# Kernel tuning notes

Hardware: AMD Instinct MI355X
Metric: run time of the kernel (lower is better)

The kernel has to match this reference:

```python
import jax, jax.numpy as jnp
import numpy as np

N_NODES = 100000
N_EDGES = 6_400_000
IN_DIM = 128


def gcn_conv(x, W, b, row, col, ew):
    """PyG GCNConv(normalize=True, add_self_loops=True) forward."""
    n = x.shape[0]
    loop = jnp.arange(n)
    row_sl = jnp.concatenate([row, loop])
    col_sl = jnp.concatenate([col, loop])
    ew_sl = jnp.concatenate([ew, jnp.ones((n,), ew.dtype)])
    # symmetric normalization: deg^{-1/2}[src] * w * deg^{-1/2}[dst]
    deg = jax.ops.segment_sum(ew_sl, col_sl, num_segments=n)
    safe_deg = jnp.where(deg > 0, deg, 1.0)
    dis = jnp.where(deg > 0, jax.lax.rsqrt(safe_deg), 0.0)
    norm = dis[row_sl] * ew_sl * dis[col_sl]
    h = x @ W  # [n, out_dim] linear transform first (small out_dim)
    # gather source features, scale, scatter-add into targets
    out = jax.ops.segment_sum(norm[:, None] * h[row_sl], col_sl, num_segments=n)
    return out + b


def setup_inputs() -> dict:
    key = jax.random.key(0)
    ks = jax.random.split(key, 12)
    X = jax.random.normal(ks[0], (N_NODES, IN_DIM), dtype=jnp.float32)
    edge_index = jax.random.randint(ks[1], (2, N_EDGES), 0, N_NODES, dtype=jnp.int64)
    edge_weight = jax.random.uniform(ks[2], (N_EDGES,), dtype=jnp.float32)

    def glorot(k, fan_in, fan_out):
        lim = np.sqrt(6.0 / (fan_in + fan_out)).astype(np.float32)
        return jax.random.uniform(k, (fan_in, fan_out), minval=-lim, maxval=lim, dtype=jnp.float32)

    return {
        "X": X,
        "edge_index": edge_index,
        "edge_weight": edge_weight,
        "W1": glorot(ks[3], IN_DIM, 12), "b1": jnp.zeros((12,), jnp.float32),
        "W2": glorot(ks[4], 12, 6), "b2": jnp.zeros((6,), jnp.float32),
        "W3": glorot(ks[5], 6, 3), "b3": jnp.zeros((3,), jnp.float32),
        "Wl": glorot(ks[6], 3, 1), "bl": jnp.zeros((1,), jnp.float32),
    }


def reference(X, edge_index, edge_weight, W1, b1, W2, b2, W3, b3, Wl, bl):
    row, col = edge_index[0], edge_index[1]
    h = jax.nn.relu(gcn_conv(X, W1, b1, row, col, edge_weight))
    # dropout p=0.2 is identity in eval mode
    h = jax.nn.relu(gcn_conv(h, W2, b2, row, col, edge_weight))
    h = jax.nn.relu(gcn_conv(h, W3, b3, row, col, edge_weight))
    out = jax.nn.sigmoid(h @ Wl + bl)
    return out.squeeze(1)  # [N]
```

## Files before the change

kernel.cpp:

```cpp
#include <hip/hip_runtime.h>
#include <cstdint>
#include <cstddef>

#define RANGE    128
#define RSHIFT   7
#define MAXBUCK  800
#define CSHIFT   12
#define CRANGE   4096
#define MAXC     32
#define FPB      32
#define CH_CNT   8192
#define CH_SC    4096
#define EPT      16
#define PAD      16
#define WSTR     132

typedef _Float16 h8 __attribute__((ext_vector_type(8)));

__global__ void zero_pad_kernel(int* __restrict__ p, int n) {
    int i = blockIdx.x * blockDim.x + threadIdx.x;
    if (i < n) p[i * PAD] = 0;
}

__global__ void count_kernel(const int* __restrict__ col, int* __restrict__ fcnt,
                             int nfine, int E) {
    __shared__ int lcnt[MAXBUCK];
    int tid = threadIdx.x;
    for (int i = tid; i < nfine; i += blockDim.x) lcnt[i] = 0;
    __syncthreads();
    int base = blockIdx.x * CH_CNT;
    int end  = min(E, base + CH_CNT);
    for (int e = base + tid; e < end; e += blockDim.x)
        atomicAdd(&lcnt[col[e] >> RSHIFT], 1);
    __syncthreads();
    for (int i = tid; i < nfine; i += blockDim.x)
        if (lcnt[i]) atomicAdd(&fcnt[i * PAD], lcnt[i]);
}

__global__ void scan_kernel(const int* __restrict__ fcnt, int* __restrict__ fbase,
                            int* __restrict__ fcur, int* __restrict__ cbase,
                            int* __restrict__ ccur, int* __restrict__ row_ptr,
                            int nfine, int ncoarse, int N, int E) {
    __shared__ int lds[1024];
    int T = threadIdx.x;
    int s = (T < nfine) ? fcnt[T * PAD] : 0;
    lds[T] = s;
    __syncthreads();
    for (int off = 1; off < 1024; off <<= 1) {
        int v = (T >= off) ? lds[T - off] : 0;
        __syncthreads();
        lds[T] += v;
        __syncthreads();
    }
    int excl = lds[T] - s;
    if (T < nfine) { fbase[T] = excl; fcur[T * PAD] = excl; }
    if ((T & (FPB - 1)) == 0 && (T >> 5) < ncoarse) {
        cbase[T >> 5] = excl;
        ccur[(T >> 5) * PAD] = excl;
    }
    if (T == 0) { fbase[nfine] = E; cbase[ncoarse] = E; row_ptr[N] = E; }
}

__global__ void coarse_scatter_kernel(const int* __restrict__ row, const int* __restrict__ col,
                                      const float* __restrict__ ew, int* __restrict__ ccur,
                                      uint2* __restrict__ partA, int ncoarse, int E) {
    __shared__ uint2 stage[CH_SC];
    __shared__ unsigned char sb[CH_SC];
    __shared__ int lcnt[MAXC], lofs[MAXC], gofs[MAXC];
    __shared__ int total_s;
    int tid = threadIdx.x;
    if (tid < MAXC) lcnt[tid] = 0;
    __syncthreads();
    int base = blockIdx.x * CH_SC;
    int cnt  = min(E - base, CH_SC);

    uint2 rec[EPT]; int rnk[EPT]; int bb[EPT];
#pragma unroll
    for (int k = 0; k < EPT; k++) {
        int idx = tid + (k << 8);
        if (idx < cnt) {
            int e = base + idx;
            int c = col[e];
            int b = c >> CSHIFT;
            bb[k]  = b;
            rec[k] = make_uint2((unsigned)row[e] | ((unsigned)(c & (CRANGE - 1)) << 17),
                                __float_as_uint(ew[e]));
            rnk[k] = atomicAdd(&lcnt[b], 1);
        }
    }
    __syncthreads();
    if (tid == 0) {
        int run = 0;
        for (int i = 0; i < ncoarse; i++) { lofs[i] = run; run += lcnt[i]; }
        total_s = run;
    }
    __syncthreads();
    if (tid < ncoarse) {
        int c = lcnt[tid];
        if (c) {
            int g = atomicAdd(&ccur[tid * PAD], c);
            gofs[tid] = g - lofs[tid];
        }
    }
#pragma unroll
    for (int k = 0; k < EPT; k++) {
        int idx = tid + (k << 8);
        if (idx < cnt) {
            int p = lofs[bb[k]] + rnk[k];
            stage[p] = rec[k];
            sb[p] = (unsigned char)bb[k];
        }
    }
    __syncthreads();
    int total = total_s;
    for (int i = tid; i < total; i += 256)
        partA[gofs[sb[i]] + i] = stage[i];
}

__global__ __launch_bounds__(256, 3)
void fine_scatter_kernel(const uint2* __restrict__ partA, const int* __restrict__ cbase,
                                    int* __restrict__ fcur, uint2* __restrict__ partB,
                                    int nfine, int ncoarse, int E) {
    __shared__ uint2 stage[CH_SC];
    __shared__ unsigned short sb[CH_SC];
    __shared__ int lcnt[MAXBUCK], lofs[MAXBUCK], gofs[MAXBUCK];
    __shared__ int tmp[256];
    __shared__ int scb[MAXC + 1];
    __shared__ int rlo_s, total_s;
    int tid = threadIdx.x;
    int base = blockIdx.x * CH_SC;
    int cnt  = min(E - base, CH_SC);
    if (tid <= ncoarse) scb[tid] = cbase[tid];
    for (int i = tid; i < nfine; i += 256) lcnt[i] = 0;
    if (tid == 0) {
        int r = 0;
        while (r < ncoarse - 1 && cbase[r + 1] <= base) ++r;
        rlo_s = r;
    }
    __syncthreads();
    int rlo = rlo_s;

    uint2 rec[EPT]; int rnk[EPT]; int ff[EPT];
#pragma unroll
    for (int k = 0; k < EPT; k++) {
        int idx = tid + (k << 8);
        if (idx < cnt) {
            int e = base + idx;
            uint2 v = partA[e];
            int r = rlo;
            while (e >= scb[r + 1]) ++r;
            int col12 = (int)((v.x >> 17) & (CRANGE - 1));
            int f = (r << 5) | (col12 >> RSHIFT);
            ff[k]  = f;
            rec[k] = make_uint2((v.x & 0x1FFFFu) | ((unsigned)(col12 & (RANGE - 1)) << 17), v.y);
            rnk[k] = atomicAdd(&lcnt[f], 1);
        }
    }
    __syncthreads();
    {
        const int Cc = (nfine + 255) >> 8;
        int b0 = tid * Cc;
        int s = 0;
        for (int i = 0; i < Cc; i++) {
            int idx = b0 + i;
            if (idx < nfine) s += lcnt[idx];
        }
        tmp[tid] = s;
        __syncthreads();
        for (int off = 1; off < 256; off <<= 1) {
            int v = (tid >= off) ? tmp[tid - off] : 0;
            __syncthreads();
            tmp[tid] += v;
            __syncthreads();
        }
        int run = tmp[tid] - s;
        for (int i = 0; i < Cc; i++) {
            int idx = b0 + i;
            if (idx < nfine) { lofs[idx] = run; run += lcnt[idx]; }
        }
        if (tid == 255) total_s = tmp[255];
    }
    __syncthreads();
    for (int i = tid; i < nfine; i += 256) {
        int c = lcnt[i];
        if (c) {
            int g = atomicAdd(&fcur[i * PAD], c);
            gofs[i] = g - lofs[i];
        }
    }
#pragma unroll
    for (int k = 0; k < EPT; k++) {
        int idx = tid + (k << 8);
        if (idx < cnt) {
            int p = lofs[ff[k]] + rnk[k];
            stage[p] = rec[k];
            sb[p] = (unsigned short)ff[k];
        }
    }
    __syncthreads();
    int total = total_s;
    for (int i = tid; i < total; i += 256)
        partB[gofs[sb[i]] + i] = stage[i];
}

__global__ void bucket_csr_kernel(const uint2* __restrict__ part, const int* __restrict__ bbase,
                                  int* __restrict__ row_ptr, float* __restrict__ dis,
                                  uint2* __restrict__ csr, int N) {
    __shared__ int   scnt[RANGE];
    __shared__ int   sscan[RANGE];
    __shared__ float sdeg[RANGE];
    __shared__ float sdis[RANGE];
    int b = blockIdx.x, tid = threadIdx.x;
    int s = bbase[b], t = bbase[b + 1];
    if (tid < RANGE) { scnt[tid] = 0; sdeg[tid] = 1.0f; }
    __syncthreads();
    for (int e = s + tid; e < t; e += blockDim.x) {
        uint2 r = part[e];
        int c = (r.x >> 17) & (RANGE - 1);
        atomicAdd(&scnt[c], 1);
        atomicAdd(&sdeg[c], __uint_as_float(r.y));
    }
    __syncthreads();
    int cnt_t = 0;
    if (tid < RANGE) { cnt_t = scnt[tid]; sscan[tid] = cnt_t; }
    __syncthreads();
    for (int off = 1; off < RANGE; off <<= 1) {
        int v = 0;
        if (tid < RANGE && tid >= off) v = sscan[tid - off];
        __syncthreads();
        if (tid < RANGE) sscan[tid] += v;
        __syncthreads();
    }
    if (tid < RANGE) {
        int excl = sscan[tid] - cnt_t;
        int node = b * RANGE + tid;
        float dn = rsqrtf(sdeg[tid]);
        sdis[tid] = dn;
        if (node < N) {
            row_ptr[node] = s + excl;
            dis[node] = dn;
        }
        scnt[tid] = excl;
    }
    __syncthreads();
    for (int e = s + tid; e < t; e += blockDim.x) {
        uint2 r = part[e];
        int c   = (r.x >> 17) & (RANGE - 1);
        int src = (int)(r.x & 0x1FFFFu);
        float v = sdis[c] * __uint_as_float(r.y);
        int off = atomicAdd(&scnt[c], 1);
        csr[s + off] = make_uint2((unsigned)src, __float_as_uint(v));
    }
}

__global__ void lin1_kernel(const float* __restrict__ X, const float* __restrict__ W1,
                            const float* __restrict__ dis, uint4* __restrict__ t1, int n) {
    __shared__ float w1t[12 * WSTR];
    int tid = threadIdx.x;
    for (int i = tid; i < 128 * 12; i += 256) {
        int k = i / 12, o = i - k * 12;
        w1t[o * WSTR + k] = W1[i];
    }
    __syncthreads();
    int gt   = blockIdx.x * 256 + tid;
    int node = gt >> 3;
    int sub  = gt & 7;
    if (node >= n) return;

    const float4* xp = (const float4*)(X + (size_t)node * 128 + sub * 16);
    float4 x0 = xp[0], x1 = xp[1], x2 = xp[2], x3 = xp[3];

    float res[12];
#pragma unroll
    for (int o = 0; o < 12; o++) {
        const float4* wp = (const float4*)(w1t + o * WSTR + sub * 16);
        float4 w0 = wp[0], w1v = wp[1], w2 = wp[2], w3 = wp[3];
        float s;
        s  = x0.x * w0.x + x0.y * w0.y + x0.z * w0.z + x0.w * w0.w;
        s += x1.x * w1v.x + x1.y * w1v.y + x1.z * w1v.z + x1.w * w1v.w;
        s += x2.x * w2.x + x2.y * w2.y + x2.z * w2.z + x2.w * w2.w;
        s += x3.x * w3.x + x3.y * w3.y + x3.z * w3.z + x3.w * w3.w;
        res[o] = s;
    }
#pragma unroll
    for (int o = 0; o < 12; o++) {
        res[o] += __shfl_xor(res[o], 1, 64);
        res[o] += __shfl_xor(res[o], 2, 64);
        res[o] += __shfl_xor(res[o], 4, 64);
    }
    if (sub == 0) {
        h8 a, b;
#pragma unroll
        for (int o = 0; o < 8; o++) a[o] = (_Float16)res[o];
#pragma unroll
        for (int o = 0; o < 4; o++) b[o] = (_Float16)res[8 + o];
#pragma unroll
        for (int o = 4; o < 8; o++) b[o] = (_Float16)0.f;
        uint4 ua = __builtin_bit_cast(uint4, a);
        uint4 ub = __builtin_bit_cast(uint4, b);
        ub.z = __float_as_uint(dis[node]);
        ub.w = 0u;
        uint4* dst = t1 + (size_t)node * 2;
        dst[0] = ua;
        dst[1] = ub;
    }
}

template <int DIN, int ROWW, int DOUT, bool LAST>
__global__ void agg_kernel(const int* __restrict__ row_ptr, const uint2* __restrict__ csr,
                           const uint4* __restrict__ hin,
                           const float* __restrict__ b_this, const float* __restrict__ W_next,
                           const float* __restrict__ b_next, void* __restrict__ hout_v, int n) {
    int gt   = blockIdx.x * blockDim.x + threadIdx.x;
    int node = gt >> 3;
    int sub  = gt & 7;
    if (node >= n) return;
    int start = row_ptr[node];
    int end   = row_ptr[node + 1];
    float acc[DIN];
#pragma unroll
    for (int d = 0; d < DIN; d++) acc[d] = 0.f;

    for (int e = start + sub; e < end; e += 8) {
        unsigned long long raw =
            __builtin_nontemporal_load((const unsigned long long*)(csr + e));
        int src    = (int)(unsigned)raw;
        float ewdd = __uint_as_float((unsigned)(raw >> 32));
        const uint4* hr = hin + (size_t)src * ROWW;
        if constexpr (DIN == 12) {
            uint4 ua = hr[0], ub = hr[1];
            float norm = ewdd * __uint_as_float(ub.z);
            h8 a = __builtin_bit_cast(h8, ua);
            h8 b = __builtin_bit_cast(h8, ub);
#pragma unroll
            for (int d = 0; d < 8; d++) acc[d] += norm * (float)a[d];
#pragma unroll
            for (int d = 0; d < 4; d++) acc[8 + d] += norm * (float)b[d];
        } else if constexpr (DIN == 6) {
            uint4 u = hr[0];
            float norm = ewdd * __uint_as_float(u.w);
            h8 a = __builtin_bit_cast(h8, u);
#pragma unroll
            for (int d = 0; d < 6; d++) acc[d] += norm * (float)a[d];
        } else {
            uint4 u = hr[0];
            float norm = ewdd * __uint_as_float(u.z);
            h8 a = __builtin_bit_cast(h8, u);
#pragma unroll
            for (int d = 0; d < 3; d++) acc[d] += norm * (float)a[d];
        }
    }

#pragma unroll
    for (int d = 0; d < DIN; d++) {
        acc[d] += __shfl_xor(acc[d], 1, 64);
        acc[d] += __shfl_xor(acc[d], 2, 64);
        acc[d] += __shfl_xor(acc[d], 4, 64);
    }

    if (sub == 0) {
        const uint4* hn = hin + (size_t)node * ROWW;
        float v[DIN];
        float dn;
        if constexpr (DIN == 12) {
            uint4 ua = hn[0], ub = hn[1];
            dn = __uint_as_float(ub.z);
            float s2 = dn * dn;
            h8 a = __builtin_bit_cast(h8, ua);
            h8 b = __builtin_bit_cast(h8, ub);
#pragma unroll
            for (int d = 0; d < 8; d++) v[d] = fmaxf(acc[d] + s2 * (float)a[d] + b_this[d], 0.f);
#pragma unroll
            for (int d = 0; d < 4; d++) v[8 + d] = fmaxf(acc[8 + d] + s2 * (float)b[d] + b_this[8 + d], 0.f);
        } else if constexpr (DIN == 6) {
            uint4 u = hn[0];
            dn = __uint_as_float(u.w);
            float s2 = dn * dn;
            h8 a = __builtin_bit_cast(h8, u);
#pragma unroll
            for (int d = 0; d < 6; d++) v[d] = fmaxf(acc[d] + s2 * (float)a[d] + b_this[d], 0.f);
        } else {
            uint4 u = hn[0];
            dn = __uint_as_float(u.z);
            float s2 = dn * dn;
            h8 a = __builtin_bit_cast(h8, u);
#pragma unroll
            for (int d = 0; d < 3; d++) v[d] = fmaxf(acc[d] + s2 * (float)a[d] + b_this[d], 0.f);
        }
        if constexpr (!LAST) {
            float o[DOUT];
#pragma unroll
            for (int oo = 0; oo < DOUT; oo++) {
                float z = 0.f;
#pragma unroll
                for (int d = 0; d < DIN; d++) z += v[d] * W_next[d * DOUT + oo];
                o[oo] = z;
            }
            h8 w;
#pragma unroll
            for (int oo = 0; oo < 8; oo++) w[oo] = (_Float16)0.f;
#pragma unroll
            for (int oo = 0; oo < DOUT; oo++) w[oo] = (_Float16)o[oo];
            uint4 uw = __builtin_bit_cast(uint4, w);
            if constexpr (DOUT == 6) uw.w = __float_as_uint(dn);
            else                     uw.z = __float_as_uint(dn);
            ((uint4*)hout_v)[node] = uw;
        } else {
            float z = b_next[0];
#pragma unroll
            for (int d = 0; d < DIN; d++) z += v[d] * W_next[d];
            ((float*)hout_v)[node] = 1.0f / (1.0f + expf(-z));
        }
    }
}

extern "C" void kernel_launch(void* const* d_in, const int* in_sizes, int n_in,
                              void* d_out, int out_size, void* d_ws, size_t ws_size,
                              hipStream_t stream) {
    const float* X  = (const float*)d_in[0];
    const int*   ei = (const int*)d_in[1];
    const float* ew = (const float*)d_in[2];
    const float* W1 = (const float*)d_in[3];
    const float* b1 = (const float*)d_in[4];
    const float* W2 = (const float*)d_in[5];
    const float* b2 = (const float*)d_in[6];
    const float* W3 = (const float*)d_in[7];
    const float* b3 = (const float*)d_in[8];
    const float* Wl = (const float*)d_in[9];
    const float* bl = (const float*)d_in[10];
    float* out = (float*)d_out;

    const int N = in_sizes[0] / 128;
    const int E = in_sizes[1] / 2;
    const int* row = ei;
    const int* col = ei + E;
    const int nfine   = (N + RANGE - 1) >> RSHIFT;
    const int ncoarse = (N + CRANGE - 1) >> CSHIFT;

    char* ws = (char*)d_ws;
    size_t off = 0;
    auto carve = [&](size_t bytes) -> void* {
        void* p = ws + off;
        off += (bytes + 255) & ~(size_t)255;
        return p;
    };
    int*   fcnt    = (int*)  carve((size_t)MAXBUCK * PAD * 4);
    int*   fcur    = (int*)  carve((size_t)MAXBUCK * PAD * 4);
    int*   ccur    = (int*)  carve((size_t)MAXC * PAD * 4);
    int*   cbase   = (int*)  carve((size_t)(MAXC + 1) * 4);
    int*   fbase   = (int*)  carve((size_t)(MAXBUCK + 1) * 4);
    int*   row_ptr = (int*)  carve((size_t)(N + 1) * 4);
    float* dis     = (float*)carve((size_t)N * 4);
    uint2* partA   = (uint2*)carve((size_t)E * 8);
    uint2* partB   = (uint2*)carve((size_t)E * 8);
    uint2* csr = partA;
    uint4* t1  = (uint4*)partB;
    uint4* t2  = t1 + (size_t)N * 2;
    uint4* t3  = t2 + (size_t)N;
    (void)ws_size; (void)n_in; (void)out_size;

    const int bCnt = (E + CH_CNT - 1) / CH_CNT;
    const int bSc  = (E + CH_SC - 1) / CH_SC;
    const int bL   = ((size_t)N * 8 + 255) / 256;
    const int bA   = ((size_t)N * 8 + 255) / 256;

    zero_pad_kernel<<<(nfine + 255) / 256, 256, 0, stream>>>(fcnt, nfine);
    count_kernel<<<bCnt, 256, 0, stream>>>(col, fcnt, nfine, E);
    scan_kernel<<<1, 1024, 0, stream>>>(fcnt, fbase, fcur, cbase, ccur, row_ptr,
                                        nfine, ncoarse, N, E);
    coarse_scatter_kernel<<<bSc, 256, 0, stream>>>(row, col, ew, ccur, partA, ncoarse, E);
    fine_scatter_kernel<<<bSc, 256, 0, stream>>>(partA, cbase, fcur, partB, nfine, ncoarse, E);
    bucket_csr_kernel<<<nfine, 256, 0, stream>>>(partB, fbase, row_ptr, dis, csr, N);
    lin1_kernel<<<bL, 256, 0, stream>>>(X, W1, dis, t1, N);
    agg_kernel<12, 2, 6, false><<<bA, 256, 0, stream>>>(row_ptr, csr, t1, b1, W2, nullptr, t2, N);
    agg_kernel< 6, 1, 3, false><<<bA, 256, 0, stream>>>(row_ptr, csr, t2, b2, W3, nullptr, t3, N);
    agg_kernel< 3, 1, 1, true ><<<bA, 256, 0, stream>>>(row_ptr, csr, t3, b3, Wl, bl, out, N);
}
```

Before: 557.4 us.

## Drop per-node CSR build; aggregate per 128-node bucket with LDS atomics

Removes the per-node CSR construction and row_ptr, keeping only a degree kernel over the fine-bucketed edge partition. Each aggregation block now owns one 128-node bucket. It streams that bucket's edges into LDS through global_load_lds chunks and accumulates features with shared-memory float atomics before the fused epilogue. This avoids a full pass that rewrites all edges into CSR order, but adds contended LDS atomics, where the old code kept register accumulators with shuffle reductions.

```diff
diff --git a/kernel.cpp b/kernel.cpp
--- a/kernel.cpp
+++ b/kernel.cpp
@@ -14,8 +14,14 @@
 #define EPT      16
 #define PAD      16
 #define WSTR     132
+#define ACHUNK   4096
 
 typedef _Float16 h8 __attribute__((ext_vector_type(8)));
+
+#define GLOAD_LDS16(gsrc, ldsb)                                                   \
+    __builtin_amdgcn_global_load_lds(                                             \
+        (const __attribute__((address_space(1))) uint32_t*)(gsrc),                \
+        (__attribute__((address_space(3))) uint32_t*)(ldsb), 16, 0, 0)
 
 __global__ void zero_pad_kernel(int* __restrict__ p, int n) {
     int i = blockIdx.x * blockDim.x + threadIdx.x;
@@ -39,8 +45,7 @@
 
 __global__ void scan_kernel(const int* __restrict__ fcnt, int* __restrict__ fbase,
                             int* __restrict__ fcur, int* __restrict__ cbase,
-                            int* __restrict__ ccur, int* __restrict__ row_ptr,
-                            int nfine, int ncoarse, int N, int E) {
+                            int* __restrict__ ccur, int nfine, int ncoarse, int E) {
     __shared__ int lds[1024];
     int T = threadIdx.x;
     int s = (T < nfine) ? fcnt[T * PAD] : 0;
@@ -58,7 +63,7 @@
         cbase[T >> 5] = excl;
         ccur[(T >> 5) * PAD] = excl;
     }
-    if (T == 0) { fbase[nfine] = E; cbase[ncoarse] = E; row_ptr[N] = E; }
+    if (T == 0) { fbase[nfine] = E; cbase[ncoarse] = E; }
 }
 
 __global__ void coarse_scatter_kernel(const int* __restrict__ row, const int* __restrict__ col,
@@ -203,53 +208,22 @@
         partB[gofs[sb[i]] + i] = stage[i];
 }
 
-__global__ void bucket_csr_kernel(const uint2* __restrict__ part, const int* __restrict__ bbase,
-                                  int* __restrict__ row_ptr, float* __restrict__ dis,
-                                  uint2* __restrict__ csr, int N) {
-    __shared__ int   scnt[RANGE];
-    __shared__ int   sscan[RANGE];
+__global__ __launch_bounds__(512)
+void deg_kernel(const uint2* __restrict__ partB, const int* __restrict__ fbase,
+                float* __restrict__ dis, int N) {
     __shared__ float sdeg[RANGE];
-    __shared__ float sdis[RANGE];
     int b = blockIdx.x, tid = threadIdx.x;
-    int s = bbase[b], t = bbase[b + 1];
-    if (tid < RANGE) { scnt[tid] = 0; sdeg[tid] = 1.0f; }
-    __syncthreads();
-    for (int e = s + tid; e < t; e += blockDim.x) {
-        uint2 r = part[e];
-        int c = (r.x >> 17) & (RANGE - 1);
-        atomicAdd(&scnt[c], 1);
-        atomicAdd(&sdeg[c], __uint_as_float(r.y));
-    }
-    __syncthreads();
-    int cnt_t = 0;
-    if (tid < RANGE) { cnt_t = scnt[tid]; sscan[tid] = cnt_t; }
-    __syncthreads();
-    for (int off = 1; off < RANGE; off <<= 1) {
-        int v = 0;
-        if (tid < RANGE && tid >= off) v = sscan[tid - off];
-        __syncthreads();
-        if (tid < RANGE) sscan[tid] += v;
-        __syncthreads();
-    }
+    int s = fbase[b], t = fbase[b + 1];
+    if (tid < RANGE) sdeg[tid] = 1.0f;
+    __syncthreads();
+    for (int e = s + tid; e < t; e += 512) {
+        uint2 r = partB[e];
+        atomicAdd(&sdeg[(r.x >> 17) & (RANGE - 1)], __uint_as_float(r.y));
+    }
+    __syncthreads();
     if (tid < RANGE) {
-        int excl = sscan[tid] - cnt_t;
         int node = b * RANGE + tid;
-        float dn = rsqrtf(sdeg[tid]);
-        sdis[tid] = dn;
-        if (node < N) {
-            row_ptr[node] = s + excl;
-            dis[node] = dn;
-        }
-        scnt[tid] = excl;
-    }
-    __syncthreads();
-    for (int e = s + tid; e < t; e += blockDim.x) {
-        uint2 r = part[e];
-        int c   = (r.x >> 17) & (RANGE - 1);
-        int src = (int)(r.x & 0x1FFFFu);
-        float v = sdis[c] * __uint_as_float(r.y);
-        int off = atomicAdd(&scnt[c], 1);
-        csr[s + off] = make_uint2((unsigned)src, __float_as_uint(v));
+        if (node < N) dis[node] = rsqrtf(sdeg[tid]);
     }
 }
 
@@ -307,109 +281,134 @@
 }
 
 template <int DIN, int ROWW, int DOUT, bool LAST>
-__global__ void agg_kernel(const int* __restrict__ row_ptr, const uint2* __restrict__ csr,
-                           const uint4* __restrict__ hin,
-                           const float* __restrict__ b_this, const float* __restrict__ W_next,
-                           const float* __restrict__ b_next, void* __restrict__ hout_v, int n) {
-    int gt   = blockIdx.x * blockDim.x + threadIdx.x;
-    int node = gt >> 3;
-    int sub  = gt & 7;
-    if (node >= n) return;
-    int start = row_ptr[node];
-    int end   = row_ptr[node + 1];
-    float acc[DIN];
-#pragma unroll
-    for (int d = 0; d < DIN; d++) acc[d] = 0.f;
-
-    for (int e = start + sub; e < end; e += 8) {
-        unsigned long long raw =
-            __builtin_nontemporal_load((const unsigned long long*)(csr + e));
-        int src    = (int)(unsigned)raw;
-        float ewdd = __uint_as_float((unsigned)(raw >> 32));
+__global__ __launch_bounds__(512, 4)
+void agg_kernel(const uint2* __restrict__ partB, const int* __restrict__ fbase,
+                const float* __restrict__ dis, const uint4* __restrict__ hin,
+                const float* __restrict__ b_this, const float* __restrict__ W_next,
+                const float* __restrict__ b_next, void* __restrict__ hout_v, int N) {
+    __shared__ uint2 stage[ACHUNK];
+    __shared__ float acc[RANGE * DIN];
+    __shared__ float sdis[RANGE];
+    int b = blockIdx.x, tid = threadIdx.x;
+    int s = fbase[b], t = fbase[b + 1];
+    int cnt = t - s;
+    for (int i = tid; i < RANGE * DIN; i += 512) acc[i] = 0.f;
+    if (tid < RANGE) {
+        int node = b * RANGE + tid;
+        sdis[tid] = (node < N) ? dis[node] : 0.f;
+    }
+
+    auto scatter1 = [&](uint2 r) {
+        int src = (int)(r.x & 0x1FFFFu);
+        int c   = (int)((r.x >> 17) & (RANGE - 1));
+        float ew = __uint_as_float(r.y);
         const uint4* hr = hin + (size_t)src * ROWW;
+        float* ac = acc + c * DIN;
         if constexpr (DIN == 12) {
             uint4 ua = hr[0], ub = hr[1];
-            float norm = ewdd * __uint_as_float(ub.z);
+            float norm = ew * __uint_as_float(ub.z) * sdis[c];
             h8 a = __builtin_bit_cast(h8, ua);
-            h8 b = __builtin_bit_cast(h8, ub);
-#pragma unroll
-            for (int d = 0; d < 8; d++) acc[d] += norm * (float)a[d];
-#pragma unroll
-            for (int d = 0; d < 4; d++) acc[8 + d] += norm * (float)b[d];
+            h8 bb = __builtin_bit_cast(h8, ub);
+#pragma unroll
+            for (int d = 0; d < 8; d++) atomicAdd(&ac[d], norm * (float)a[d]);
+#pragma unroll
+            for (int d = 0; d < 4; d++) atomicAdd(&ac[8 + d], norm * (float)bb[d]);
         } else if constexpr (DIN == 6) {
             uint4 u = hr[0];
-            float norm = ewdd * __uint_as_float(u.w);
+            float norm = ew * __uint_as_float(u.w) * sdis[c];
             h8 a = __builtin_bit_cast(h8, u);
 #pragma unroll
-            for (int d = 0; d < 6; d++) acc[d] += norm * (float)a[d];
+            for (int d = 0; d < 6; d++) atomicAdd(&ac[d], norm * (float)a[d]);
         } else {
             uint4 u = hr[0];
-            float norm = ewdd * __uint_as_float(u.z);
+            float norm = ew * __uint_as_float(u.z) * sdis[c];
             h8 a = __builtin_bit_cast(h8, u);
 #pragma unroll
-            for (int d = 0; d < 3; d++) acc[d] += norm * (float)a[d];
-        }
-    }
-
-#pragma unroll
-    for (int d = 0; d < DIN; d++) {
-        acc[d] += __shfl_xor(acc[d], 1, 64);
-        acc[d] += __shfl_xor(acc[d], 2, 64);
-        acc[d] += __shfl_xor(acc[d], 4, 64);
-    }
-
-    if (sub == 0) {
-        const uint4* hn = hin + (size_t)node * ROWW;
-        float v[DIN];
-        float dn;
-        if constexpr (DIN == 12) {
-            uint4 ua = hn[0], ub = hn[1];
-            dn = __uint_as_float(ub.z);
+            for (int d = 0; d < 3; d++) atomicAdd(&ac[d], norm * (float)a[d]);
+        }
+    };
+
+    int nch = (cnt + ACHUNK - 1) / ACHUNK;
+    for (int ch = 0; ch < nch; ++ch) {
+        int cb  = ch * ACHUNK;
+        int clim = min(cnt - cb, ACHUNK);
+        {
+            int wave = tid >> 6, lane = tid & 63;
+            int iters = (clim + 1023) >> 10;
+            for (int it = 0; it < iters; ++it) {
+                int rb = (it << 10) + (wave << 7);
+                const uint2* src = partB + s + cb + rb + (lane << 1);
+                GLOAD_LDS16(src, (char*)stage + ((size_t)rb << 3));
+            }
+        }
+        asm volatile("s_waitcnt vmcnt(0)" ::: "memory");
+        __syncthreads();
+        int i = tid;
+        for (; i + 512 < clim; i += 1024) {
+            uint2 r0 = stage[i];
+            uint2 r1 = stage[i + 512];
+            scatter1(r0);
+            scatter1(r1);
+        }
+        if (i < clim) scatter1(stage[i]);
+        __syncthreads();
+    }
+    __syncthreads();
+
+    if (tid < RANGE) {
+        int node = b * RANGE + tid;
+        if (node < N) {
+            const uint4* hn = hin + (size_t)node * ROWW;
+            float dn = sdis[tid];
             float s2 = dn * dn;
-            h8 a = __builtin_bit_cast(h8, ua);
-            h8 b = __builtin_bit_cast(h8, ub);
-#pragma unroll
-            for (int d = 0; d < 8; d++) v[d] = fmaxf(acc[d] + s2 * (float)a[d] + b_this[d], 0.f);
-#pragma unroll
-            for (int d = 0; d < 4; d++) v[8 + d] = fmaxf(acc[8 + d] + s2 * (float)b[d] + b_this[8 + d], 0.f);
-        } else if constexpr (DIN == 6) {
-            uint4 u = hn[0];
-            dn = __uint_as_float(u.w);
-            float s2 = dn * dn;
-            h8 a = __builtin_bit_cast(h8, u);
-#pragma unroll
-            for (int d = 0; d < 6; d++) v[d] = fmaxf(acc[d] + s2 * (float)a[d] + b_this[d], 0.f);
-        } else {
-            uint4 u = hn[0];
-            dn = __uint_as_float(u.z);
-            float s2 = dn * dn;
-            h8 a = __builtin_bit_cast(h8, u);
-#pragma unroll
-            for (int d = 0; d < 3; d++) v[d] = fmaxf(acc[d] + s2 * (float)a[d] + b_this[d], 0.f);
-        }
-        if constexpr (!LAST) {
-            float o[DOUT];
-#pragma unroll
-            for (int oo = 0; oo < DOUT; oo++) {
-                float z = 0.f;
-#pragma unroll
-                for (int d = 0; d < DIN; d++) z += v[d] * W_next[d * DOUT + oo];
-                o[oo] = z;
+            float v[DIN];
+            if constexpr (DIN == 12) {
+                uint4 ua = hn[0], ub = hn[1];
+                h8 a = __builtin_bit_cast(h8, ua);
+                h8 bb = __builtin_bit_cast(h8, ub);
+#pragma unroll
+                for (int d = 0; d < 8; d++)
+                    v[d] = fmaxf(acc[tid * DIN + d] + s2 * (float)a[d] + b_this[d], 0.f);
+#pragma unroll
+                for (int d = 0; d < 4; d++)
+                    v[8 + d] = fmaxf(acc[tid * DIN + 8 + d] + s2 * (float)bb[d] + b_this[8 + d], 0.f);
+            } else if constexpr (DIN == 6) {
+                uint4 u = hn[0];
+                h8 a = __builtin_bit_cast(h8, u);
+#pragma unroll
+                for (int d = 0; d < 6; d++)
+                    v[d] = fmaxf(acc[tid * DIN + d] + s2 * (float)a[d] + b_this[d], 0.f);
+            } else {
+                uint4 u = hn[0];
+                h8 a = __builtin_bit_cast(h8, u);
+#pragma unroll
+                for (int d = 0; d < 3; d++)
+                    v[d] = fmaxf(acc[tid * DIN + d] + s2 * (float)a[d] + b_this[d], 0.f);
             }
-            h8 w;
-#pragma unroll
-            for (int oo = 0; oo < 8; oo++) w[oo] = (_Float16)0.f;
-#pragma unroll
-            for (int oo = 0; oo < DOUT; oo++) w[oo] = (_Float16)o[oo];
-            uint4 uw = __builtin_bit_cast(uint4, w);
-            if constexpr (DOUT == 6) uw.w = __float_as_uint(dn);
-            else                     uw.z = __float_as_uint(dn);
-            ((uint4*)hout_v)[node] = uw;
-        } else {
-            float z = b_next[0];
-#pragma unroll
-            for (int d = 0; d < DIN; d++) z += v[d] * W_next[d];
-            ((float*)hout_v)[node] = 1.0f / (1.0f + expf(-z));
+            if constexpr (!LAST) {
+                float o[DOUT];
+#pragma unroll
+                for (int oo = 0; oo < DOUT; oo++) {
+                    float z = 0.f;
+#pragma unroll
+                    for (int d = 0; d < DIN; d++) z += v[d] * W_next[d * DOUT + oo];
+                    o[oo] = z;
+                }
+                h8 w;
+#pragma unroll
+                for (int oo = 0; oo < 8; oo++) w[oo] = (_Float16)0.f;
+#pragma unroll
+                for (int oo = 0; oo < DOUT; oo++) w[oo] = (_Float16)o[oo];
+                uint4 uw = __builtin_bit_cast(uint4, w);
+                if constexpr (DOUT == 6) uw.w = __float_as_uint(dn);
+                else                     uw.z = __float_as_uint(dn);
+                ((uint4*)hout_v)[node] = uw;
+            } else {
+                float z = b_next[0];
+#pragma unroll
+                for (int d = 0; d < DIN; d++) z += v[d] * W_next[d];
+                ((float*)hout_v)[node] = 1.0f / (1.0f + expf(-z));
+            }
         }
     }
 }
@@ -449,12 +448,10 @@
     int*   ccur    = (int*)  carve((size_t)MAXC * PAD * 4);
     int*   cbase   = (int*)  carve((size_t)(MAXC + 1) * 4);
     int*   fbase   = (int*)  carve((size_t)(MAXBUCK + 1) * 4);
-    int*   row_ptr = (int*)  carve((size_t)(N + 1) * 4);
     float* dis     = (float*)carve((size_t)N * 4);
     uint2* partA   = (uint2*)carve((size_t)E * 8);
-    uint2* partB   = (uint2*)carve((size_t)E * 8);
-    uint2* csr = partA;
-    uint4* t1  = (uint4*)partB;
+    uint2* partB   = (uint2*)carve((size_t)(E + 1024) * 8);
+    uint4* t1  = (uint4*)partA;
     uint4* t2  = t1 + (size_t)N * 2;
     uint4* t3  = t2 + (size_t)N;
     (void)ws_size; (void)n_in; (void)out_size;
@@ -462,17 +459,16 @@
     const int bCnt = (E + CH_CNT - 1) / CH_CNT;
     const int bSc  = (E + CH_SC - 1) / CH_SC;
     const int bL   = ((size_t)N * 8 + 255) / 256;
-    const int bA   = ((size_t)N * 8 + 255) / 256;
 
     zero_pad_kernel<<<(nfine + 255) / 256, 256, 0, stream>>>(fcnt, nfine);
     count_kernel<<<bCnt, 256, 0, stream>>>(col, fcnt, nfine, E);
-    scan_kernel<<<1, 1024, 0, stream>>>(fcnt, fbase, fcur, cbase, ccur, row_ptr,
-                                        nfine, ncoarse, N, E);
+    scan_kernel<<<1, 1024, 0, stream>>>(fcnt, fbase, fcur, cbase, ccur,
+                                        nfine, ncoarse, E);
     coarse_scatter_kernel<<<bSc, 256, 0, stream>>>(row, col, ew, ccur, partA, ncoarse, E);
     fine_scatter_kernel<<<bSc, 256, 0, stream>>>(partA, cbase, fcur, partB, nfine, ncoarse, E);
-    bucket_csr_kernel<<<nfine, 256, 0, stream>>>(partB, fbase, row_ptr, dis, csr, N);
+    deg_kernel<<<nfine, 512, 0, stream>>>(partB, fbase, dis, N);
     lin1_kernel<<<bL, 256, 0, stream>>>(X, W1, dis, t1, N);
-    agg_kernel<12, 2, 6, false><<<bA, 256, 0, stream>>>(row_ptr, csr, t1, b1, W2, nullptr, t2, N);
-    agg_kernel< 6, 1, 3, false><<<bA, 256, 0, stream>>>(row_ptr, csr, t2, b2, W3, nullptr, t3, N);
-    agg_kernel< 3, 1, 1, true ><<<bA, 256, 0, stream>>>(row_ptr, csr, t3, b3, Wl, bl, out, N);
-}
+    agg_kernel<12, 2, 6, false><<<nfine, 512, 0, stream>>>(partB, fbase, dis, t1, b1, W2, nullptr, t2, N);
+    agg_kernel< 6, 1, 3, false><<<nfine, 512, 0, stream>>>(partB, fbase, dis, t2, b2, W3, nullptr, t3, N);
+    agg_kernel< 3, 1, 1, true ><<<nfine, 512, 0, stream>>>(partB, fbase, dis, t3, b3, Wl, bl, out, N);
+}
```

Result: slower. 1.239 ms (+122.3%).
